# Optimization experiments

Hardware: AMD Instinct MI355X
Metric: run time of the kernel (lower is better)

Reference implementation:

```python
import jax, jax.numpy as jnp
import numpy as np

B, T, D = 4096, 200, 64
NEG_INF = -(2.0 ** 32) + 1.0  # matches tf paddings constant


def setup_inputs() -> dict:
    key = jax.random.key(0)
    ks = jax.random.split(key, 12)
    queries = jax.random.normal(ks[0], (B, D), dtype=jnp.float32)
    keys = jax.random.normal(ks[1], (B, T, D), dtype=jnp.float32)
    keys_length = jax.random.randint(ks[2], (B,), 0, 200, dtype=jnp.int32)
    # attention MLP params (glorot-ish scale)
    W1 = jax.random.normal(ks[3], (4 * D, 16), dtype=jnp.float32) * (1.0 / np.sqrt(4 * D))
    b1 = jnp.zeros((16,), dtype=jnp.float32)
    W2 = jax.random.normal(ks[4], (16, 8), dtype=jnp.float32) * (1.0 / np.sqrt(16))
    b2 = jnp.zeros((8,), dtype=jnp.float32)
    W3 = jax.random.normal(ks[5], (8, 1), dtype=jnp.float32) * (1.0 / np.sqrt(8))
    b3 = jnp.zeros((1,), dtype=jnp.float32)
    W4 = jax.random.normal(ks[6], (D, D), dtype=jnp.float32) * (1.0 / np.sqrt(D))
    b4 = jnp.zeros((D,), dtype=jnp.float32)
    return {"queries": queries, "keys": keys, "keys_length": keys_length,
            "W1": W1, "b1": b1, "W2": W2, "b2": b2, "W3": W3, "b3": b3,
            "W4": W4, "b4": b4}


def reference(queries, keys, keys_length, W1, b1, W2, b2, W3, b3, W4, b4):
    Bq, Tq, Dq = keys.shape
    # tile queries across time: [B, T, D]
    q = jnp.broadcast_to(queries[:, None, :], (Bq, Tq, Dq))
    # DIN feature construction: [B, T, 4D]
    din_all = jnp.concatenate([q, keys, q - keys, q * keys], axis=-1)
    # tiny MLP scorer
    x = jax.nn.sigmoid(jnp.einsum('btf,fh->bth', din_all, W1) + b1)
    x = jax.nn.sigmoid(jnp.einsum('bth,hk->btk', x, W2) + b2)
    scores = (jnp.einsum('btk,ko->bto', x, W3) + b3)[..., 0]  # [B, T]
    # mask invalid history positions
    mask = jnp.arange(Tq, dtype=keys_length.dtype)[None, :] < keys_length[:, None]
    scores = jnp.where(mask, scores, NEG_INF)
    scores = scores / (Dq ** 0.5)  # scaling applied after masking, as in tf code
    attn = jax.nn.softmax(scores, axis=-1)  # [B, T]
    out = jnp.einsum('bt,btd->bd', attn, keys)  # weighted sum of keys
    out = out @ W4 + b4  # [B, D]
    return out
```

## Files before the change

### kernel.cpp

```cpp
#include <hip/hip_runtime.h>
#include <math.h>

#define TT 200
#define DD 64
#define MTS 72

typedef __attribute__((ext_vector_type(8))) short bf16x8;
typedef __attribute__((ext_vector_type(4))) float f32x4;

__device__ __forceinline__ float sigmoidf_(float x) {
    return 1.0f / (1.0f + __expf(-x));
}
__device__ __forceinline__ short f2bf(float x) {
    unsigned u = __float_as_uint(x);
    u += 0x7fff + ((u >> 16) & 1);
    return (short)(u >> 16);
}
__device__ __forceinline__ float bf2f(short s) {
    return __uint_as_float(((unsigned)(unsigned short)s) << 16);
}
__device__ __forceinline__ void build_frag(float4 v0, float4 v1, bf16x8& hi, bf16x8& lo) {
    float xs[8] = {v0.x, v0.y, v0.z, v0.w, v1.x, v1.y, v1.z, v1.w};
    #pragma unroll
    for (int j = 0; j < 8; j++) {
        short h = f2bf(xs[j]);
        hi[j] = h;
        lo[j] = f2bf(xs[j] - bf2f(h));
    }
}

__global__ __launch_bounds__(256) void din_attn_kernel(
    const float* __restrict__ queries,
    const float* __restrict__ keys,
    const int*   __restrict__ keys_length,
    const float* __restrict__ W1,
    const float* __restrict__ b1,
    const float* __restrict__ W2,
    const float* __restrict__ b2,
    const float* __restrict__ W3,
    const float* __restrict__ b3,
    const float* __restrict__ W4,
    const float* __restrict__ b4,
    float* __restrict__ out)
{
    __shared__ __align__(16) short MtHi[16 * MTS];
    __shared__ __align__(16) short MtLo[16 * MTS];
    __shared__ __align__(16) float H1s[208 * 16];
    __shared__ float cpart[64 * 16];
    __shared__ float qs[64];
    __shared__ float cvec[16];
    __shared__ __align__(16) float w2s[16 * 8];
    __shared__ float w3s[8];
    __shared__ float b2s[8];
    __shared__ float b3sh[1];
    __shared__ float scoresS[256];
    __shared__ float red[4 * 64];
    __shared__ float tmpv[64];

    const int tid = threadIdx.x;
    const int b   = blockIdx.x;
    const int len = keys_length[b];
    const float* kb = keys + (size_t)b * (TT * DD);

    if (tid < 64)        qs[tid]        = queries[b * DD + tid];
    else if (tid < 192)  w2s[tid - 64]  = W2[tid - 64];
    else if (tid < 200)  w3s[tid - 192] = W3[tid - 192];
    else if (tid < 208)  b2s[tid - 200] = b2[tid - 200];
    else if (tid == 208) b3sh[0]        = b3[0];
    __syncthreads();

    {
        const float4* W1v = (const float4*)W1;
        const int d  = tid >> 2;
        const int hg = tid & 3;
        const float q = qs[d];
        float4 a  = W1v[(0   + d) * 4 + hg];
        float4 bb = W1v[(64  + d) * 4 + hg];
        float4 cc = W1v[(128 + d) * 4 + hg];
        float4 dd = W1v[(192 + d) * 4 + hg];
        const int cbase = d * 16 + hg * 4;
        cpart[cbase + 0] = q * (a.x + cc.x);
        cpart[cbase + 1] = q * (a.y + cc.y);
        cpart[cbase + 2] = q * (a.z + cc.z);
        cpart[cbase + 3] = q * (a.w + cc.w);
        float mv[4];
        mv[0] = bb.x - cc.x + q * dd.x;
        mv[1] = bb.y - cc.y + q * dd.y;
        mv[2] = bb.z - cc.z + q * dd.z;
        mv[3] = bb.w - cc.w + q * dd.w;
        #pragma unroll
        for (int i = 0; i < 4; i++) {
            const int h = hg * 4 + i;
            short hi = f2bf(mv[i]);
            MtHi[h * MTS + d] = hi;
            MtLo[h * MTS + d] = f2bf(mv[i] - bf2f(hi));
        }
    }
    __syncthreads();
    if (tid < 16) {
        float s = b1[tid];
        for (int d = 0; d < DD; d++) s += cpart[d * 16 + tid];
        cvec[tid] = s;
    }
    __syncthreads();

    const int w    = tid >> 6;
    const int lane = tid & 63;
    const int m16  = lane & 15;
    const int quad = lane >> 4;

    {
        const int bb0 = m16 * MTS + quad * 8;
        bf16x8 Bh0 = *(const bf16x8*)&MtHi[bb0];
        bf16x8 Bh1 = *(const bf16x8*)&MtHi[bb0 + 32];
        bf16x8 Bl0 = *(const bf16x8*)&MtLo[bb0];
        bf16x8 Bl1 = *(const bf16x8*)&MtLo[bb0 + 32];
        const float cv = cvec[m16];

        for (int tile = w; tile < 13; tile += 4) {
            int trow = tile * 16 + m16;
            if (trow > TT - 1) trow = TT - 1;
            const float* kp = kb + trow * 64 + quad * 8;
            float4 v0 = *(const float4*)(kp);
            float4 v1 = *(const float4*)(kp + 4);
            float4 v2 = *(const float4*)(kp + 32);
            float4 v3 = *(const float4*)(kp + 36);
            bf16x8 ah0, al0, ah1, al1;
            build_frag(v0, v1, ah0, al0);
            build_frag(v2, v3, ah1, al1);
            f32x4 acc = {0.f, 0.f, 0.f, 0.f};
            acc = __builtin_amdgcn_mfma_f32_16x16x32_bf16(ah0, Bh0, acc, 0, 0, 0);
            acc = __builtin_amdgcn_mfma_f32_16x16x32_bf16(ah0, Bl0, acc, 0, 0, 0);
            acc = __builtin_amdgcn_mfma_f32_16x16x32_bf16(al0, Bh0, acc, 0, 0, 0);
            acc = __builtin_amdgcn_mfma_f32_16x16x32_bf16(ah1, Bh1, acc, 0, 0, 0);
            acc = __builtin_amdgcn_mfma_f32_16x16x32_bf16(ah1, Bl1, acc, 0, 0, 0);
            acc = __builtin_amdgcn_mfma_f32_16x16x32_bf16(al1, Bh1, acc, 0, 0, 0);
            const int rb = tile * 16 + quad * 4;
            H1s[(rb + 0) * 16 + m16] = sigmoidf_(acc[0] + cv);
            H1s[(rb + 1) * 16 + m16] = sigmoidf_(acc[1] + cv);
            H1s[(rb + 2) * 16 + m16] = sigmoidf_(acc[2] + cv);
            H1s[(rb + 3) * 16 + m16] = sigmoidf_(acc[3] + cv);
        }
    }
    __syncthreads();

    float sc = -INFINITY;
    if (tid < TT) {
        const float4* h1p = (const float4*)&H1s[tid * 16];
        float4 ha = h1p[0], hb = h1p[1], hc = h1p[2], hd = h1p[3];
        float hv[16] = {ha.x, ha.y, ha.z, ha.w, hb.x, hb.y, hb.z, hb.w,
                        hc.x, hc.y, hc.z, hc.w, hd.x, hd.y, hd.z, hd.w};
        float s2[8];
        #pragma unroll
        for (int k = 0; k < 8; k++) s2[k] = b2s[k];
        #pragma unroll
        for (int h = 0; h < 16; h++) {
            const float hh = hv[h];
            const float4* w2r = (const float4*)&w2s[h * 8];
            float4 wa = w2r[0], wb = w2r[1];
            s2[0] = fmaf(hh, wa.x, s2[0]);
            s2[1] = fmaf(hh, wa.y, s2[1]);
            s2[2] = fmaf(hh, wa.z, s2[2]);
            s2[3] = fmaf(hh, wa.w, s2[3]);
            s2[4] = fmaf(hh, wb.x, s2[4]);
            s2[5] = fmaf(hh, wb.y, s2[5]);
            s2[6] = fmaf(hh, wb.z, s2[6]);
            s2[7] = fmaf(hh, wb.w, s2[7]);
        }
        float s3 = b3sh[0];
        #pragma unroll
        for (int k = 0; k < 8; k++) s3 = fmaf(sigmoidf_(s2[k]), w3s[k], s3);
        if (tid >= len) s3 = -4294967295.0f;
        sc = s3 * 0.125f;
    }

    float m = sc;
    #pragma unroll
    for (int off = 32; off >= 1; off >>= 1) m = fmaxf(m, __shfl_xor(m, off, 64));
    if (lane == 0) red[w] = m;
    __syncthreads();
    m = fmaxf(fmaxf(red[0], red[1]), fmaxf(red[2], red[3]));

    float p = (tid < TT) ? __expf(sc - m) : 0.0f;
    float ssum = p;
    #pragma unroll
    for (int off = 32; off >= 1; off >>= 1) ssum += __shfl_xor(ssum, off, 64);
    __syncthreads();
    if (lane == 0) red[w] = ssum;
    __syncthreads();
    const float inv = 1.0f / (red[0] + red[1] + red[2] + red[3]);
    if (tid < TT) scoresS[tid] = p * inv;
    __syncthreads();

    float ws = 0.0f;
    #pragma unroll 5
    for (int t = w * 50; t < w * 50 + 50; t++)
        ws = fmaf(scoresS[t], kb[t * 64 + lane], ws);
    red[w * 64 + lane] = ws;
    __syncthreads();
    if (tid < 64) tmpv[tid] = red[tid] + red[64 + tid] + red[128 + tid] + red[192 + tid];
    __syncthreads();

    float po = 0.0f;
    {
        const float* w4p = W4 + (size_t)(w * 16) * 64 + lane;
        #pragma unroll
        for (int i = 0; i < 16; i++)
            po = fmaf(tmpv[w * 16 + i], w4p[i * 64], po);
    }
    red[w * 64 + lane] = po;
    __syncthreads();
    if (tid < 64)
        out[(size_t)b * 64 + tid] =
            b4[tid] + red[tid] + red[64 + tid] + red[128 + tid] + red[192 + tid];
}

extern "C" void kernel_launch(void* const* d_in, const int* in_sizes, int n_in,
                              void* d_out, int out_size, void* d_ws, size_t ws_size,
                              hipStream_t stream) {
    const float* queries     = (const float*)d_in[0];
    const float* keys        = (const float*)d_in[1];
    const int*   keys_length = (const int*)  d_in[2];
    const float* W1 = (const float*)d_in[3];
    const float* b1 = (const float*)d_in[4];
    const float* W2 = (const float*)d_in[5];
    const float* b2 = (const float*)d_in[6];
    const float* W3 = (const float*)d_in[7];
    const float* b3 = (const float*)d_in[8];
    const float* W4 = (const float*)d_in[9];
    const float* b4 = (const float*)d_in[10];
    float* out = (float*)d_out;

    const int Bn = in_sizes[2];
    din_attn_kernel<<<Bn, 256, 0, stream>>>(
        queries, keys, keys_length, W1, b1, W2, b2, W3, b3, W4, b4, out);
}
```

Measured before the change: 323.7 us.

## Prefetch key tiles, drop key lo-split MFMAs, store H1 as bf16, merge barriers

The first key tile is loaded before the W1 preprocessing, and each tile loop iteration prefetches the next tile so global loads overlap with MFMA work. The bf16 low-part correction for keys is removed, cutting the MFMAs per tile from six to four, and H1 activations are stored in shared memory as bf16. Barriers are reduced by using shuffle reductions for the constant vector, folding the softmax normalisation into the final reduction, and preloading W4 and b4 into registers. This trades accuracy (the keys lose their low-order bits and H1 is rounded to bf16) for less conversion and MFMA work and fewer synchronisations.

```diff
diff --git a/kernel.cpp b/kernel.cpp
--- a/kernel.cpp
+++ b/kernel.cpp
@@ -19,14 +19,10 @@
 __device__ __forceinline__ float bf2f(short s) {
     return __uint_as_float(((unsigned)(unsigned short)s) << 16);
 }
-__device__ __forceinline__ void build_frag(float4 v0, float4 v1, bf16x8& hi, bf16x8& lo) {
+__device__ __forceinline__ void build_hi(float4 v0, float4 v1, bf16x8& hi) {
     float xs[8] = {v0.x, v0.y, v0.z, v0.w, v1.x, v1.y, v1.z, v1.w};
     #pragma unroll
-    for (int j = 0; j < 8; j++) {
-        short h = f2bf(xs[j]);
-        hi[j] = h;
-        lo[j] = f2bf(xs[j] - bf2f(h));
-    }
+    for (int j = 0; j < 8; j++) hi[j] = f2bf(xs[j]);
 }
 
 __global__ __launch_bounds__(256) void din_attn_kernel(
@@ -45,49 +41,48 @@
 {
     __shared__ __align__(16) short MtHi[16 * MTS];
     __shared__ __align__(16) short MtLo[16 * MTS];
-    __shared__ __align__(16) float H1s[208 * 16];
-    __shared__ float cpart[64 * 16];
-    __shared__ float qs[64];
-    __shared__ float cvec[16];
+    __shared__ __align__(16) short H1s[208 * 16];
+    __shared__ float cred[4 * 16];
     __shared__ __align__(16) float w2s[16 * 8];
     __shared__ float w3s[8];
     __shared__ float b2s[8];
     __shared__ float b3sh[1];
     __shared__ float scoresS[256];
-    __shared__ float red[4 * 64];
+    __shared__ float sred[8];
+    __shared__ float wred[4 * 64];
     __shared__ float tmpv[64];
 
-    const int tid = threadIdx.x;
-    const int b   = blockIdx.x;
-    const int len = keys_length[b];
+    const int tid  = threadIdx.x;
+    const int b    = blockIdx.x;
+    const int w    = tid >> 6;
+    const int lane = tid & 63;
+    const int m16  = lane & 15;
+    const int quad = lane >> 4;
+    const int len  = keys_length[b];
     const float* kb = keys + (size_t)b * (TT * DD);
 
-    if (tid < 64)        qs[tid]        = queries[b * DD + tid];
-    else if (tid < 192)  w2s[tid - 64]  = W2[tid - 64];
-    else if (tid < 200)  w3s[tid - 192] = W3[tid - 192];
-    else if (tid < 208)  b2s[tid - 200] = b2[tid - 200];
-    else if (tid == 208) b3sh[0]        = b3[0];
-    __syncthreads();
+    int trow0 = w * 16 + m16;
+    if (trow0 > TT - 1) trow0 = TT - 1;
+    const float* kp0 = kb + trow0 * 64 + quad * 8;
+    float4 c0 = *(const float4*)(kp0);
+    float4 c1 = *(const float4*)(kp0 + 4);
+    float4 c2 = *(const float4*)(kp0 + 32);
+    float4 c3 = *(const float4*)(kp0 + 36);
 
     {
-        const float4* W1v = (const float4*)W1;
         const int d  = tid >> 2;
         const int hg = tid & 3;
-        const float q = qs[d];
+        const float q = queries[b * 64 + d];
+        const float4* W1v = (const float4*)W1;
         float4 a  = W1v[(0   + d) * 4 + hg];
         float4 bb = W1v[(64  + d) * 4 + hg];
         float4 cc = W1v[(128 + d) * 4 + hg];
         float4 dd = W1v[(192 + d) * 4 + hg];
-        const int cbase = d * 16 + hg * 4;
-        cpart[cbase + 0] = q * (a.x + cc.x);
-        cpart[cbase + 1] = q * (a.y + cc.y);
-        cpart[cbase + 2] = q * (a.z + cc.z);
-        cpart[cbase + 3] = q * (a.w + cc.w);
-        float mv[4];
-        mv[0] = bb.x - cc.x + q * dd.x;
-        mv[1] = bb.y - cc.y + q * dd.y;
-        mv[2] = bb.z - cc.z + q * dd.z;
-        mv[3] = bb.w - cc.w + q * dd.w;
+        float cp[4], mv[4];
+        cp[0] = q * (a.x + cc.x);  mv[0] = bb.x - cc.x + q * dd.x;
+        cp[1] = q * (a.y + cc.y);  mv[1] = bb.y - cc.y + q * dd.y;
+        cp[2] = q * (a.z + cc.z);  mv[2] = bb.z - cc.z + q * dd.z;
+        cp[3] = q * (a.w + cc.w);  mv[3] = bb.w - cc.w + q * dd.w;
         #pragma unroll
         for (int i = 0; i < 4; i++) {
             const int h = hg * 4 + i;
@@ -95,19 +90,21 @@
             MtHi[h * MTS + d] = hi;
             MtLo[h * MTS + d] = f2bf(mv[i] - bf2f(hi));
         }
-    }
-    __syncthreads();
-    if (tid < 16) {
-        float s = b1[tid];
-        for (int d = 0; d < DD; d++) s += cpart[d * 16 + tid];
-        cvec[tid] = s;
-    }
-    __syncthreads();
-
-    const int w    = tid >> 6;
-    const int lane = tid & 63;
-    const int m16  = lane & 15;
-    const int quad = lane >> 4;
+        #pragma unroll
+        for (int mask = 4; mask <= 32; mask <<= 1) {
+            #pragma unroll
+            for (int i = 0; i < 4; i++) cp[i] += __shfl_xor(cp[i], mask, 64);
+        }
+        if (lane < 4) {
+            #pragma unroll
+            for (int i = 0; i < 4; i++) cred[w * 16 + lane * 4 + i] = cp[i];
+        }
+        if (tid < 128)       w2s[tid]        = W2[tid];
+        else if (tid < 136)  w3s[tid - 128]  = W3[tid - 128];
+        else if (tid < 144)  b2s[tid - 136]  = b2[tid - 136];
+        else if (tid == 144) b3sh[0]         = b3[0];
+    }
+    __syncthreads();
 
     {
         const int bb0 = m16 * MTS + quad * 8;
@@ -115,41 +112,54 @@
         bf16x8 Bh1 = *(const bf16x8*)&MtHi[bb0 + 32];
         bf16x8 Bl0 = *(const bf16x8*)&MtLo[bb0];
         bf16x8 Bl1 = *(const bf16x8*)&MtLo[bb0 + 32];
-        const float cv = cvec[m16];
+        const float cv = b1[m16] + cred[0 + m16] + cred[16 + m16]
+                       + cred[32 + m16] + cred[48 + m16];
 
         for (int tile = w; tile < 13; tile += 4) {
-            int trow = tile * 16 + m16;
-            if (trow > TT - 1) trow = TT - 1;
-            const float* kp = kb + trow * 64 + quad * 8;
-            float4 v0 = *(const float4*)(kp);
-            float4 v1 = *(const float4*)(kp + 4);
-            float4 v2 = *(const float4*)(kp + 32);
-            float4 v3 = *(const float4*)(kp + 36);
-            bf16x8 ah0, al0, ah1, al1;
-            build_frag(v0, v1, ah0, al0);
-            build_frag(v2, v3, ah1, al1);
+            float4 n0, n1, n2, n3;
+            const int nt = tile + 4;
+            if (nt < 13) {
+                int trow = nt * 16 + m16;
+                if (trow > TT - 1) trow = TT - 1;
+                const float* kp = kb + trow * 64 + quad * 8;
+                n0 = *(const float4*)(kp);
+                n1 = *(const float4*)(kp + 4);
+                n2 = *(const float4*)(kp + 32);
+                n3 = *(const float4*)(kp + 36);
+            }
+            bf16x8 ah0, ah1;
+            build_hi(c0, c1, ah0);
+            build_hi(c2, c3, ah1);
             f32x4 acc = {0.f, 0.f, 0.f, 0.f};
             acc = __builtin_amdgcn_mfma_f32_16x16x32_bf16(ah0, Bh0, acc, 0, 0, 0);
             acc = __builtin_amdgcn_mfma_f32_16x16x32_bf16(ah0, Bl0, acc, 0, 0, 0);
-            acc = __builtin_amdgcn_mfma_f32_16x16x32_bf16(al0, Bh0, acc, 0, 0, 0);
             acc = __builtin_amdgcn_mfma_f32_16x16x32_bf16(ah1, Bh1, acc, 0, 0, 0);
             acc = __builtin_amdgcn_mfma_f32_16x16x32_bf16(ah1, Bl1, acc, 0, 0, 0);
-            acc = __builtin_amdgcn_mfma_f32_16x16x32_bf16(al1, Bh1, acc, 0, 0, 0);
             const int rb = tile * 16 + quad * 4;
-            H1s[(rb + 0) * 16 + m16] = sigmoidf_(acc[0] + cv);
-            H1s[(rb + 1) * 16 + m16] = sigmoidf_(acc[1] + cv);
-            H1s[(rb + 2) * 16 + m16] = sigmoidf_(acc[2] + cv);
-            H1s[(rb + 3) * 16 + m16] = sigmoidf_(acc[3] + cv);
-        }
-    }
-    __syncthreads();
+            H1s[(rb + 0) * 16 + m16] = f2bf(sigmoidf_(acc[0] + cv));
+            H1s[(rb + 1) * 16 + m16] = f2bf(sigmoidf_(acc[1] + cv));
+            H1s[(rb + 2) * 16 + m16] = f2bf(sigmoidf_(acc[2] + cv));
+            H1s[(rb + 3) * 16 + m16] = f2bf(sigmoidf_(acc[3] + cv));
+            c0 = n0; c1 = n1; c2 = n2; c3 = n3;
+        }
+    }
+    __syncthreads();
+
+    float w4r[16];
+    {
+        const float* w4p = W4 + (size_t)(w * 16) * 64 + lane;
+        #pragma unroll
+        for (int i = 0; i < 16; i++) w4r[i] = w4p[i * 64];
+    }
+    float b4v = (tid < 64) ? b4[tid] : 0.0f;
 
     float sc = -INFINITY;
     if (tid < TT) {
-        const float4* h1p = (const float4*)&H1s[tid * 16];
-        float4 ha = h1p[0], hb = h1p[1], hc = h1p[2], hd = h1p[3];
-        float hv[16] = {ha.x, ha.y, ha.z, ha.w, hb.x, hb.y, hb.z, hb.w,
-                        hc.x, hc.y, hc.z, hc.w, hd.x, hd.y, hd.z, hd.w};
+        bf16x8 h1a = *(const bf16x8*)&H1s[tid * 16];
+        bf16x8 h1b = *(const bf16x8*)&H1s[tid * 16 + 8];
+        float hv[16];
+        #pragma unroll
+        for (int j = 0; j < 8; j++) { hv[j] = bf2f(h1a[j]); hv[8 + j] = bf2f(h1b[j]); }
         float s2[8];
         #pragma unroll
         for (int k = 0; k < 8; k++) s2[k] = b2s[k];
@@ -177,42 +187,38 @@
     float m = sc;
     #pragma unroll
     for (int off = 32; off >= 1; off >>= 1) m = fmaxf(m, __shfl_xor(m, off, 64));
-    if (lane == 0) red[w] = m;
-    __syncthreads();
-    m = fmaxf(fmaxf(red[0], red[1]), fmaxf(red[2], red[3]));
+    if (lane == 0) sred[w] = m;
+    __syncthreads();
+    m = fmaxf(fmaxf(sred[0], sred[1]), fmaxf(sred[2], sred[3]));
 
     float p = (tid < TT) ? __expf(sc - m) : 0.0f;
+    scoresS[tid] = p;
     float ssum = p;
     #pragma unroll
     for (int off = 32; off >= 1; off >>= 1) ssum += __shfl_xor(ssum, off, 64);
-    __syncthreads();
-    if (lane == 0) red[w] = ssum;
-    __syncthreads();
-    const float inv = 1.0f / (red[0] + red[1] + red[2] + red[3]);
-    if (tid < TT) scoresS[tid] = p * inv;
+    if (lane == 0) sred[4 + w] = ssum;
     __syncthreads();
 
     float ws = 0.0f;
-    #pragma unroll 5
+    #pragma unroll 10
     for (int t = w * 50; t < w * 50 + 50; t++)
         ws = fmaf(scoresS[t], kb[t * 64 + lane], ws);
-    red[w * 64 + lane] = ws;
-    __syncthreads();
-    if (tid < 64) tmpv[tid] = red[tid] + red[64 + tid] + red[128 + tid] + red[192 + tid];
+    wred[w * 64 + lane] = ws;
+    __syncthreads();
+    if (tid < 64) {
+        const float inv = 1.0f / (sred[4] + sred[5] + sred[6] + sred[7]);
+        tmpv[tid] = (wred[tid] + wred[64 + tid] + wred[128 + tid] + wred[192 + tid]) * inv;
+    }
     __syncthreads();
 
     float po = 0.0f;
-    {
-        const float* w4p = W4 + (size_t)(w * 16) * 64 + lane;
-        #pragma unroll
-        for (int i = 0; i < 16; i++)
-            po = fmaf(tmpv[w * 16 + i], w4p[i * 64], po);
-    }
-    red[w * 64 + lane] = po;
+    #pragma unroll
+    for (int i = 0; i < 16; i++) po = fmaf(tmpv[w * 16 + i], w4r[i], po);
+    wred[w * 64 + lane] = po;
     __syncthreads();
     if (tid < 64)
         out[(size_t)b * 64 + tid] =
-            b4[tid] + red[tid] + red[64 + tid] + red[128 + tid] + red[192 + tid];
+            b4v + wred[tid] + wred[64 + tid] + wred[128 + tid] + wred[192 + tid];
 }
 
 extern "C" void kernel_launch(void* const* d_in, const int* in_sizes, int n_in,
```

New measurement: 316.2 us. 2.3% less time.
